# Kernel tuning notes

Hardware: AMD Instinct MI355X
Metric: run time of the kernel (lower is better)

## Reference

```python
import jax, jax.numpy as jnp
import numpy as np

N = 50000   # nodes
E = 800000  # edges (avg degree 16)
H = 128     # hidden


def setup_inputs() -> dict:
    key = jax.random.key(0)
    k1, k2, k3, k4, k5 = jax.random.split(key, 5)
    s = 1.0 / np.sqrt(H).astype(np.float32)
    x = jax.random.normal(k1, (N, H), dtype=jnp.float32)
    edge_index = jax.random.randint(k2, (2, E), 0, N, dtype=jnp.int64)
    a_i = jax.random.normal(k3, (H,), dtype=jnp.float32) * s
    a_j = jax.random.normal(k4, (H,), dtype=jnp.float32) * s
    W = jax.random.normal(k5, (H, H), dtype=jnp.float32) * s
    return {"x": x, "edge_index": edge_index, "a_i": a_i, "a_j": a_j, "W": W}


def reference(x, edge_index, a_i, a_j, W):
    n = x.shape[0]
    idx_j = edge_index[0]  # row of sparse adj (output node)
    idx_i = edge_index[1]  # col of sparse adj (source node, softmax segment)

    # per-node attention scores, gathered per edge
    si = x @ a_i  # [N]
    sj = x @ a_j  # [N]
    e = jax.nn.leaky_relu(si[idx_i] + sj[idx_j], negative_slope=0.01)  # [E]

    # segment softmax over idx_i (numerically stable)
    seg_max = jax.ops.segment_max(e, idx_i, num_segments=n)
    e_exp = jnp.exp(e - seg_max[idx_i])
    denom = jax.ops.segment_sum(e_exp, idx_i, num_segments=n)
    alpha = e_exp / denom[idx_i]  # [E]

    # messages and sparse aggregation: out[j] += alpha * m[i]
    m = x + x @ W  # [N, H]
    out = jax.ops.segment_sum(alpha[:, None] * m[idx_i], idx_j, num_segments=n)

    # exact (erf) GELU to match torch nn.GELU default; dropout is identity in eval
    return jax.nn.gelu(out, approximate=False)
```

## Files before the change

kernel.cpp:

```cpp
#include <hip/hip_runtime.h>
#include <math.h>

#define HDIM 128
#define NB   32
#define CAP  768
#define BINB 256

typedef __attribute__((ext_vector_type(8))) short short8;
typedef __attribute__((ext_vector_type(4))) float f32x4;

__device__ __forceinline__ float gelu_f(float v) {
    return 0.5f * v * (1.0f + erff(v * 0.70710678118654752440f));
}
__device__ __forceinline__ unsigned bf_rne(float f) {
    unsigned u = __float_as_uint(f);
    return (u + 0x7fffu + ((u >> 16) & 1u)) >> 16;
}
__device__ __forceinline__ float bf_lo(unsigned u) {
    return __uint_as_float(u << 16);
}
__device__ __forceinline__ float bf_hi(unsigned u) {
    return __uint_as_float(u & 0xffff0000u);
}

__global__ void __launch_bounds__(256) k_scores(
    const float* __restrict__ x, const float* __restrict__ a_i,
    const float* __restrict__ a_j, float* __restrict__ si,
    float* __restrict__ sj, unsigned* __restrict__ xbp,
    unsigned* __restrict__ gcnt, float* __restrict__ denom, int N) {
    if (blockIdx.x == 0)
        for (int w = threadIdx.x; w < 2048; w += 256) gcnt[w] = 0u;
    const int wave = threadIdx.x >> 6;
    const int lane = threadIdx.x & 63;
    const int n = blockIdx.x * 4 + wave;
    if (n >= N) return;
    const float xa = x[(size_t)n * HDIM + lane];
    const float xb = x[(size_t)n * HDIM + 64 + lane];
    xbp[(size_t)n * 64 + lane] = bf_rne(xa) | (bf_rne(xb) << 16);
    float vi = xa * a_i[lane] + xb * a_i[64 + lane];
    float vj = xa * a_j[lane] + xb * a_j[64 + lane];
    #pragma unroll
    for (int d = 32; d; d >>= 1) {
        vi += __shfl_xor(vi, d, 64);
        vj += __shfl_xor(vj, d, 64);
    }
    if (lane == 0) {
        si[n] = vi;
        sj[n] = vj;
        denom[n] = 0.f;
    }
}

__global__ void __launch_bounds__(1024) k_bin(
    const int* __restrict__ idx_i, const int* __restrict__ idx_j,
    const float* __restrict__ si, const float* __restrict__ sj,
    float* __restrict__ denom, unsigned* __restrict__ gcnt,
    uint2* __restrict__ edges, int nbuk, int E_) {
    __shared__ unsigned cnt_l[2048];
    const int blk = blockIdx.x;
    const int chunk = (E_ + BINB - 1) / BINB;
    const int e0 = blk * chunk;
    const int e1 = min(e0 + chunk, E_);
    for (int w = threadIdx.x; w < nbuk; w += 1024) cnt_l[w] = 0u;
    __syncthreads();
    uint2 rec[4];
    int   bl[4];
    #pragma unroll
    for (int k = 0; k < 4; ++k) {
        const int t = e0 + threadIdx.x + k * 1024;
        bl[k] = -1;
        if (t < e1) {
            const int i = idx_i[t];
            const int j = idx_j[t];
            float e = si[i] + sj[j];
            e = (e > 0.f) ? e : 0.01f * e;
            const float ex = __expf(e);
            atomicAdd(&denom[i], ex);
            const int b = j >> 5;
            atomicAdd(&cnt_l[b], 1u);
            rec[k] = make_uint2((unsigned)i | ((unsigned)(j & 31) << 24),
                                __float_as_uint(ex));
            bl[k] = b;
        }
    }
    for (int t = e0 + threadIdx.x + 4 * 1024; t < e1; t += 1024) {
        const int i = idx_i[t];
        const int j = idx_j[t];
        float e = si[i] + sj[j];
        e = (e > 0.f) ? e : 0.01f * e;
        const float ex = __expf(e);
        atomicAdd(&denom[i], ex);
        const int b = j >> 5;
        const unsigned slot = min(atomicAdd(&gcnt[b], 1u), (unsigned)(CAP - 1));
        edges[(size_t)b * CAP + slot] = make_uint2(
            (unsigned)i | ((unsigned)(j & 31) << 24), __float_as_uint(ex));
    }
    __syncthreads();
    for (int w = threadIdx.x; w < nbuk; w += 1024) {
        const unsigned c = cnt_l[w];
        cnt_l[w] = c ? atomicAdd(&gcnt[w], c) : 0u;
    }
    __syncthreads();
    #pragma unroll
    for (int k = 0; k < 4; ++k) {
        if (bl[k] >= 0) {
            const unsigned slot =
                min(atomicAdd(&cnt_l[bl[k]], 1u), (unsigned)(CAP - 1));
            edges[(size_t)bl[k] * CAP + slot] = rec[k];
        }
    }
}

__global__ void __launch_bounds__(256) k_gemm(
    const unsigned* __restrict__ xbp, const float* __restrict__ Wm,
    const float* __restrict__ denom, unsigned* __restrict__ mbp, int N) {
    __shared__ unsigned wl[128][68];
    const int t = threadIdx.x;
    {
        const int n = t & 127;
        const int h = t >> 7;
        for (int w = h * 32; w < h * 32 + 32; ++w) {
            const float f0 = Wm[w * 128 + n];
            const float f1 = Wm[(w + 64) * 128 + n];
            wl[n][w] = bf_rne(f0) | (bf_rne(f1) << 16);
        }
    }
    __syncthreads();
    const int wave = t >> 6;
    const int lane = t & 63;
    const int q = lane >> 4;
    const int m16 = lane & 15;
    const int r0 = blockIdx.x * 64 + wave * 16;
    if (r0 >= N) return;
    const int rowA = min(r0 + m16, N - 1);
    union { uint4 u; short8 s; } a[4];
    #pragma unroll
    for (int kb = 0; kb < 4; ++kb)
        a[kb].u = *(const uint4*)(xbp + (size_t)rowA * 64 + kb * 16 + q * 4);
    f32x4 acc[8];
    #pragma unroll
    for (int c = 0; c < 8; ++c) acc[c] = (f32x4){0.f, 0.f, 0.f, 0.f};
    #pragma unroll
    for (int kb = 0; kb < 4; ++kb) {
        #pragma unroll
        for (int c = 0; c < 8; ++c) {
            const short8 bfr =
                *(const short8*)&wl[c * 16 + m16][kb * 16 + q * 4];
            acc[c] = __builtin_amdgcn_mfma_f32_16x16x32_bf16(
                a[kb].s, bfr, acc[c], 0, 0, 0);
        }
    }
    #pragma unroll
    for (int r = 0; r < 4; ++r) {
        const int row = r0 + q * 4 + r;
        if (row >= N) continue;
        const float rdv = 1.0f / denom[row];
        #pragma unroll
        for (int c = 0; c < 4; ++c) {
            const int w = m16 + 16 * c;
            const unsigned xv = xbp[(size_t)row * 64 + w];
            const float vlo = (bf_lo(xv) + acc[c][r]) * rdv;
            const float vhi = (bf_hi(xv) + acc[c + 4][r]) * rdv;
            mbp[(size_t)row * 64 + w] = bf_rne(vlo) | (bf_rne(vhi) << 16);
        }
    }
}

__global__ void __launch_bounds__(512) k_agg(
    const unsigned* __restrict__ gcnt, const uint2* __restrict__ edges,
    const unsigned* __restrict__ mbp, float* __restrict__ out, int N) {
    __shared__ uint2 srec[CAP];
    __shared__ unsigned cnt_l[NB];
    __shared__ unsigned off_l[NB];
    const int b = blockIdx.x;
    const int cntb = min((int)gcnt[b], CAP);
    const uint2* eb = edges + (size_t)b * CAP;
    if (threadIdx.x < NB) cnt_l[threadIdx.x] = 0u;
    __syncthreads();
    uint2 r0_ = make_uint2(0u, 0u), r1_ = make_uint2(0u, 0u);
    int jl0 = -1, jl1 = -1, kl0 = 0, kl1 = 0;
    {
        const int t0 = threadIdx.x;
        if (t0 < cntb) {
            r0_ = eb[t0];
            jl0 = (int)(r0_.x >> 24);
            kl0 = (int)atomicAdd(&cnt_l[jl0], 1u);
        }
        const int t1 = threadIdx.x + 512;
        if (t1 < cntb) {
            r1_ = eb[t1];
            jl1 = (int)(r1_.x >> 24);
            kl1 = (int)atomicAdd(&cnt_l[jl1], 1u);
        }
    }
    __syncthreads();
    if (threadIdx.x < NB) {
        const unsigned v = cnt_l[threadIdx.x];
        unsigned s = v;
        #pragma unroll
        for (int d = 1; d < NB; d <<= 1) {
            const unsigned o = __shfl_up(s, d, 64);
            if ((int)threadIdx.x >= d) s += o;
        }
        off_l[threadIdx.x] = s - v;
    }
    __syncthreads();
    if (jl0 >= 0) srec[off_l[jl0] + kl0] = r0_;
    if (jl1 >= 0) srec[off_l[jl1] + kl1] = r1_;
    __syncthreads();
    const int wave = threadIdx.x >> 6;
    const int lane = threadIdx.x & 63;
    for (int nr = wave; nr < NB; nr += 8) {
        const int n = (b << 5) + nr;
        if (n >= N) continue;
        const int p0 = (int)off_l[nr];
        const int p1 = p0 + (int)cnt_l[nr];
        float ax = 0.f, ay = 0.f;
        int p = p0;
        for (; p + 8 <= p1; p += 8) {
            const uint2 e0 = srec[p];
            const uint2 e1 = srec[p + 1];
            const uint2 e2 = srec[p + 2];
            const uint2 e3 = srec[p + 3];
            const uint2 e4 = srec[p + 4];
            const uint2 e5 = srec[p + 5];
            const uint2 e6 = srec[p + 6];
            const uint2 e7 = srec[p + 7];
            const unsigned u0 = mbp[(size_t)(e0.x & 0xffffffu) * 64 + lane];
            const unsigned u1 = mbp[(size_t)(e1.x & 0xffffffu) * 64 + lane];
            const unsigned u2 = mbp[(size_t)(e2.x & 0xffffffu) * 64 + lane];
            const unsigned u3 = mbp[(size_t)(e3.x & 0xffffffu) * 64 + lane];
            const unsigned u4 = mbp[(size_t)(e4.x & 0xffffffu) * 64 + lane];
            const unsigned u5 = mbp[(size_t)(e5.x & 0xffffffu) * 64 + lane];
            const unsigned u6 = mbp[(size_t)(e6.x & 0xffffffu) * 64 + lane];
            const unsigned u7 = mbp[(size_t)(e7.x & 0xffffffu) * 64 + lane];
            ax = fmaf(__uint_as_float(e0.y), bf_lo(u0), ax);
            ay = fmaf(__uint_as_float(e0.y), bf_hi(u0), ay);
            ax = fmaf(__uint_as_float(e1.y), bf_lo(u1), ax);
            ay = fmaf(__uint_as_float(e1.y), bf_hi(u1), ay);
            ax = fmaf(__uint_as_float(e2.y), bf_lo(u2), ax);
            ay = fmaf(__uint_as_float(e2.y), bf_hi(u2), ay);
            ax = fmaf(__uint_as_float(e3.y), bf_lo(u3), ax);
            ay = fmaf(__uint_as_float(e3.y), bf_hi(u3), ay);
            ax = fmaf(__uint_as_float(e4.y), bf_lo(u4), ax);
            ay = fmaf(__uint_as_float(e4.y), bf_hi(u4), ay);
            ax = fmaf(__uint_as_float(e5.y), bf_lo(u5), ax);
            ay = fmaf(__uint_as_float(e5.y), bf_hi(u5), ay);
            ax = fmaf(__uint_as_float(e6.y), bf_lo(u6), ax);
            ay = fmaf(__uint_as_float(e6.y), bf_hi(u6), ay);
            ax = fmaf(__uint_as_float(e7.y), bf_lo(u7), ax);
            ay = fmaf(__uint_as_float(e7.y), bf_hi(u7), ay);
        }
        for (; p + 4 <= p1; p += 4) {
            const uint2 e0 = srec[p];
            const uint2 e1 = srec[p + 1];
            const uint2 e2 = srec[p + 2];
            const uint2 e3 = srec[p + 3];
            const unsigned u0 = mbp[(size_t)(e0.x & 0xffffffu) * 64 + lane];
            const unsigned u1 = mbp[(size_t)(e1.x & 0xffffffu) * 64 + lane];
            const unsigned u2 = mbp[(size_t)(e2.x & 0xffffffu) * 64 + lane];
            const unsigned u3 = mbp[(size_t)(e3.x & 0xffffffu) * 64 + lane];
            ax = fmaf(__uint_as_float(e0.y), bf_lo(u0), ax);
            ay = fmaf(__uint_as_float(e0.y), bf_hi(u0), ay);
            ax = fmaf(__uint_as_float(e1.y), bf_lo(u1), ax);
            ay = fmaf(__uint_as_float(e1.y), bf_hi(u1), ay);
            ax = fmaf(__uint_as_float(e2.y), bf_lo(u2), ax);
            ay = fmaf(__uint_as_float(e2.y), bf_hi(u2), ay);
            ax = fmaf(__uint_as_float(e3.y), bf_lo(u3), ax);
            ay = fmaf(__uint_as_float(e3.y), bf_hi(u3), ay);
        }
        for (; p < p1; ++p) {
            const uint2 e = srec[p];
            const unsigned u = mbp[(size_t)(e.x & 0xffffffu) * 64 + lane];
            const float a = __uint_as_float(e.y);
            ax = fmaf(a, bf_lo(u), ax);
            ay = fmaf(a, bf_hi(u), ay);
        }
        out[(size_t)n * HDIM + lane] = gelu_f(ax);
        out[(size_t)n * HDIM + 64 + lane] = gelu_f(ay);
    }
}

extern "C" void kernel_launch(void* const* d_in, const int* in_sizes, int n_in,
                              void* d_out, int out_size, void* d_ws,
                              size_t ws_size, hipStream_t stream) {
    const float* x   = (const float*)d_in[0];
    const int*   eix = (const int*)d_in[1];
    const float* a_i = (const float*)d_in[2];
    const float* a_j = (const float*)d_in[3];
    const float* Wm  = (const float*)d_in[4];
    float* out = (float*)d_out;

    const int N = in_sizes[0] / HDIM;
    const int E = in_sizes[1] / 2;
    const int nbuk = (N + NB - 1) / NB;

    unsigned* xbp  = (unsigned*)d_ws;
    unsigned* mbp  = xbp + (size_t)N * 64;
    float* si      = (float*)(mbp + (size_t)N * 64);
    float* sj      = si + N;
    float* denom   = sj + N;
    unsigned* gcnt = (unsigned*)(denom + N);
    uint2* edges   = (uint2*)(gcnt + 2048);

    const int* idx_j = eix;
    const int* idx_i = eix + E;

    k_scores<<<(N + 3) / 4, 256, 0, stream>>>(x, a_i, a_j, si, sj, xbp, gcnt,
                                              denom, N);
    k_bin<<<BINB, 1024, 0, stream>>>(idx_i, idx_j, si, sj, denom, gcnt, edges,
                                     nbuk, E);
    k_gemm<<<(N + 63) / 64, 256, 0, stream>>>(xbp, Wm, denom, mbp, N);
    k_agg<<<nbuk, 512, 0, stream>>>(gcnt, edges, mbp, out, N);
}
```

Baseline: 182.4 us.

## Replace global denominator atomics with windowed shared-memory histogram and partial reduction

Each edge's exp score is now stored as fp16 in a per-edge buffer instead of being atomically added into a global denom array. A new kernel, run on 64 blocks, builds shared-memory histograms over four node windows to produce per-block partial denominators. A second new kernel sums those partials per node. The aim is to remove contended global float atomics, at the cost of two extra launches, repeated idx_i reads, a 64×N partial buffer and reduced precision from the fp16 exp values.

```diff
diff --git a/kernel.cpp b/kernel.cpp
--- a/kernel.cpp
+++ b/kernel.cpp
@@ -1,10 +1,13 @@
 #include <hip/hip_runtime.h>
+#include <hip/hip_fp16.h>
 #include <math.h>
 
 #define HDIM 128
 #define NB   32
 #define CAP  768
 #define BINB 256
+#define DG   64
+#define WIN  12544
 
 typedef __attribute__((ext_vector_type(8))) short short8;
 typedef __attribute__((ext_vector_type(4))) float f32x4;
@@ -27,7 +30,7 @@
     const float* __restrict__ x, const float* __restrict__ a_i,
     const float* __restrict__ a_j, float* __restrict__ si,
     float* __restrict__ sj, unsigned* __restrict__ xbp,
-    unsigned* __restrict__ gcnt, float* __restrict__ denom, int N) {
+    unsigned* __restrict__ gcnt, int N) {
     if (blockIdx.x == 0)
         for (int w = threadIdx.x; w < 2048; w += 256) gcnt[w] = 0u;
     const int wave = threadIdx.x >> 6;
@@ -47,14 +50,13 @@
     if (lane == 0) {
         si[n] = vi;
         sj[n] = vj;
-        denom[n] = 0.f;
     }
 }
 
 __global__ void __launch_bounds__(1024) k_bin(
     const int* __restrict__ idx_i, const int* __restrict__ idx_j,
     const float* __restrict__ si, const float* __restrict__ sj,
-    float* __restrict__ denom, unsigned* __restrict__ gcnt,
+    unsigned short* __restrict__ exbuf, unsigned* __restrict__ gcnt,
     uint2* __restrict__ edges, int nbuk, int E_) {
     __shared__ unsigned cnt_l[2048];
     const int blk = blockIdx.x;
@@ -75,7 +77,7 @@
             float e = si[i] + sj[j];
             e = (e > 0.f) ? e : 0.01f * e;
             const float ex = __expf(e);
-            atomicAdd(&denom[i], ex);
+            exbuf[t] = __half_as_ushort(__float2half(ex));
             const int b = j >> 5;
             atomicAdd(&cnt_l[b], 1u);
             rec[k] = make_uint2((unsigned)i | ((unsigned)(j & 31) << 24),
@@ -89,7 +91,7 @@
         float e = si[i] + sj[j];
         e = (e > 0.f) ? e : 0.01f * e;
         const float ex = __expf(e);
-        atomicAdd(&denom[i], ex);
+        exbuf[t] = __half_as_ushort(__float2half(ex));
         const int b = j >> 5;
         const unsigned slot = min(atomicAdd(&gcnt[b], 1u), (unsigned)(CAP - 1));
         edges[(size_t)b * CAP + slot] = make_uint2(
@@ -109,6 +111,41 @@
             edges[(size_t)bl[k] * CAP + slot] = rec[k];
         }
     }
+}
+
+__global__ void __launch_bounds__(1024) k_den(
+    const int* __restrict__ idx_i, const unsigned short* __restrict__ exbuf,
+    float* __restrict__ denp, int N, int E_) {
+    __shared__ float dl[WIN];
+    const int b = blockIdx.x;
+    const int chunk = (E_ + DG - 1) / DG;
+    const int e0 = b * chunk;
+    const int e1 = min(e0 + chunk, E_);
+    for (int pass = 0; pass < 4; ++pass) {
+        const int lo = pass * WIN;
+        for (int w = threadIdx.x; w < WIN; w += 1024) dl[w] = 0.f;
+        __syncthreads();
+        for (int t = e0 + threadIdx.x; t < e1; t += 1024) {
+            const int i = idx_i[t];
+            const unsigned rel = (unsigned)(i - lo);
+            if (rel < (unsigned)WIN)
+                atomicAdd(&dl[rel], __half2float(__ushort_as_half(exbuf[t])));
+        }
+        __syncthreads();
+        for (int w = threadIdx.x; w < WIN && lo + w < N; w += 1024)
+            denp[(size_t)b * N + lo + w] = dl[w];
+        __syncthreads();
+    }
+}
+
+__global__ void __launch_bounds__(256) k_denred(const float* __restrict__ denp,
+                                                float* __restrict__ denom,
+                                                int N) {
+    const int v = blockIdx.x * 256 + threadIdx.x;
+    if (v >= N) return;
+    float s = 0.f;
+    for (int b = 0; b < DG; ++b) s += denp[(size_t)b * N + v];
+    denom[v] = s;
 }
 
 __global__ void __launch_bounds__(256) k_gemm(
@@ -297,19 +334,23 @@
 
     unsigned* xbp  = (unsigned*)d_ws;
     unsigned* mbp  = xbp + (size_t)N * 64;
-    float* si      = (float*)(mbp + (size_t)N * 64);
+    float* denp    = (float*)(mbp + (size_t)N * 64);
+    float* si      = denp + (size_t)DG * N;
     float* sj      = si + N;
     float* denom   = sj + N;
     unsigned* gcnt = (unsigned*)(denom + N);
-    uint2* edges   = (uint2*)(gcnt + 2048);
+    unsigned short* exbuf = (unsigned short*)(gcnt + 2048);
+    uint2* edges   = (uint2*)(exbuf + ((E + 7) & ~7));
 
     const int* idx_j = eix;
     const int* idx_i = eix + E;
 
     k_scores<<<(N + 3) / 4, 256, 0, stream>>>(x, a_i, a_j, si, sj, xbp, gcnt,
-                                              denom, N);
-    k_bin<<<BINB, 1024, 0, stream>>>(idx_i, idx_j, si, sj, denom, gcnt, edges,
+                                              N);
+    k_bin<<<BINB, 1024, 0, stream>>>(idx_i, idx_j, si, sj, exbuf, gcnt, edges,
                                      nbuk, E);
+    k_den<<<DG, 1024, 0, stream>>>(idx_i, exbuf, denp, N, E);
+    k_denred<<<(N + 255) / 256, 256, 0, stream>>>(denp, denom, N);
     k_gemm<<<(N + 63) / 64, 256, 0, stream>>>(xbp, Wm, denom, mbp, N);
     k_agg<<<nbuk, 512, 0, stream>>>(gcnt, edges, mbp, out, N);
 }
```

Result: no change. 180.7 us (-0.9%).
